# Optimization experiments

Measured on AMD Instinct MI355X. Metric: run time of the kernel, lower is better.

The kernel has to match this reference:

```python
import jax, jax.numpy as jnp
import numpy as np

N = 100000
E = 1000000
F_IN = 128
HID = 64
HEADS = 4
NC = 4


def setup_inputs() -> dict:
    key = jax.random.key(0)
    ks = jax.random.split(key, 24)
    s = 0.05
    inp = {
        "x": jax.random.normal(ks[0], (N, F_IN), jnp.float32),
        "edge_index": jax.random.randint(ks[1], (2, E), 0, N, jnp.int64 if jax.config.jax_enable_x64 else jnp.int32),
        "edge_weight": jax.random.uniform(ks[2], (E,), jnp.float32),
        "node_mask": jnp.ones((N,), jnp.bool_),
        # GCNConv: lin (no bias applied pre-propagate in math below; bias added after)
        "gcn_W": s * jax.random.normal(ks[3], (F_IN, HID), jnp.float32),
        "gcn_b": jnp.zeros((HID,), jnp.float32),
        "proj_W": s * jax.random.normal(ks[4], (F_IN, HID), jnp.float32),
        "proj_b": jnp.zeros((HID,), jnp.float32),
        "ln1_g": jnp.ones((HID,), jnp.float32), "ln1_b": jnp.zeros((HID,), jnp.float32),
        # GATv2Conv heads=4, concat=False: lin_l, lin_r -> [F, H*C], att [H, C], bias [C]
        "gat_Wl": s * jax.random.normal(ks[5], (HID, HEADS * HID), jnp.float32),
        "gat_Wr": s * jax.random.normal(ks[6], (HID, HEADS * HID), jnp.float32),
        "gat_att": s * jax.random.normal(ks[7], (HEADS, HID), jnp.float32),
        "gat_b": jnp.zeros((HID,), jnp.float32),
        "ln2_g": jnp.ones((HID,), jnp.float32), "ln2_b": jnp.zeros((HID,), jnp.float32),
        # SAGEConv: lin_l (neighbors, with bias), lin_r (root, no bias)
        "sage_Wl": s * jax.random.normal(ks[8], (HID, HID), jnp.float32),
        "sage_bl": jnp.zeros((HID,), jnp.float32),
        "sage_Wr": s * jax.random.normal(ks[9], (HID, HID), jnp.float32),
        "ln3_g": jnp.ones((HID,), jnp.float32), "ln3_b": jnp.zeros((HID,), jnp.float32),
        # edge MLP: Linear(2*HID+1, 32) -> ReLU -> Linear(32, 1)
        "emlp_W1": s * jax.random.normal(ks[10], (2 * HID + 1, 32), jnp.float32),
        "emlp_b1": jnp.zeros((32,), jnp.float32),
        "emlp_W2": s * jax.random.normal(ks[11], (32, 1), jnp.float32),
        "emlp_b2": jnp.zeros((1,), jnp.float32),
        # heads on JK-cat dim 3*HID
        "mort_W": s * jax.random.normal(ks[12], (3 * HID, 1), jnp.float32),
        "mort_b": jnp.zeros((1,), jnp.float32),
        "hours_W": s * jax.random.normal(ks[13], (3 * HID, 1), jnp.float32),
        "hours_b": jnp.zeros((1,), jnp.float32),
        "disc_W": s * jax.random.normal(ks[14], (3 * HID, NC), jnp.float32),
        "disc_b": jnp.zeros((NC,), jnp.float32),
    }
    return inp


def _ln(h, g, b, eps=1e-5):
    mu = jnp.mean(h, axis=-1, keepdims=True)
    var = jnp.mean(jnp.square(h - mu), axis=-1, keepdims=True)
    return (h - mu) * jax.lax.rsqrt(var + eps) * g + b


def reference(x, edge_index, edge_weight, node_mask,
              gcn_W, gcn_b, proj_W, proj_b, ln1_g, ln1_b,
              gat_Wl, gat_Wr, gat_att, gat_b, ln2_g, ln2_b,
              sage_Wl, sage_bl, sage_Wr, ln3_g, ln3_b,
              emlp_W1, emlp_b1, emlp_W2, emlp_b2,
              mort_W, mort_b, hours_W, hours_b, disc_W, disc_b):
    n = x.shape[0]
    src, dst = edge_index[0], edge_index[1]
    loop = jnp.arange(n, dtype=src.dtype)
    s2 = jnp.concatenate([src, loop])  # edges + self loops (GCN, GATv2)
    d2 = jnp.concatenate([dst, loop])

    # ---- GCNConv (normalized, self loops with weight 1) ----
    w2 = jnp.concatenate([edge_weight, jnp.ones((n,), x.dtype)])
    deg = jax.ops.segment_sum(w2, d2, num_segments=n)
    dinv = jnp.where(deg > 0, jax.lax.rsqrt(deg), 0.0)
    norm = dinv[s2] * w2 * dinv[d2]
    xw = x @ gcn_W  # [N, HID]
    gcn_out = jax.ops.segment_sum(norm[:, None] * xw[s2], d2, num_segments=n) + gcn_b
    h1 = jax.nn.relu(_ln(gcn_out, ln1_g, ln1_b))
    h_init = h1 + (x @ proj_W + proj_b)

    # ---- edge-gated edge MLP (recomputed weights; unused by later convs, kept for fidelity) ----
    feat = jnp.concatenate([h_init[src], h_init[dst], edge_weight[:, None]], axis=1)
    _new_ew = jax.nn.sigmoid((jax.nn.relu(feat @ emlp_W1 + emlp_b1) @ emlp_W2 + emlp_b2)[:, 0])

    # ---- GATv2Conv (heads=4, concat=False -> mean over heads, self loops) ----
    H, C = gat_att.shape
    xl = (h_init @ gat_Wl).reshape(n, H, C)
    xr = (h_init @ gat_Wr).reshape(n, H, C)
    e = jax.nn.leaky_relu(xl[s2] + xr[d2], 0.2)        # [E+N, H, C]
    score = jnp.einsum('ehc,hc->eh', e, gat_att)        # [E+N, H]
    smax = jax.ops.segment_max(score, d2, num_segments=n)
    ex = jnp.exp(score - smax[d2])
    den = jax.ops.segment_sum(ex, d2, num_segments=n)
    alpha = ex / den[d2]
    gat_out = jax.ops.segment_sum(alpha[:, :, None] * xl[s2], d2, num_segments=n)
    gat_out = jnp.mean(gat_out, axis=1) + gat_b
    h2 = jax.nn.relu(_ln(gat_out, ln2_g, ln2_b)) + h_init

    # ---- SAGEConv (mean aggregation, root weight, no self loops) ----
    nsum = jax.ops.segment_sum(h2[src], dst, num_segments=n)
    cnt = jax.ops.segment_sum(jnp.ones(src.shape, h2.dtype), dst, num_segments=n)
    nmean = nsum / jnp.maximum(cnt, 1.0)[:, None]
    sage_out = nmean @ sage_Wl + sage_bl + h2 @ sage_Wr
    h3 = jax.nn.relu(_ln(sage_out, ln3_g, ln3_b)) + h2

    # ---- JumpingKnowledge cat + masked readout + heads ----
    x_jk = jnp.concatenate([h_init, h2, h3], axis=1)  # [N, 3*HID]
    readout = jnp.where(node_mask[:, None], x_jk, 0.0)
    mort = (readout @ mort_W + mort_b)[:, 0]
    hours = (readout @ hours_W + hours_b)[:, 0]
    disc = readout @ disc_W + disc_b
    return mort, hours, disc
```

## Files before the change

### kernel.cpp

```cpp
#include <hip/hip_runtime.h>
#include <hip/hip_fp16.h>
#include <math.h>

#define N_NODES 100000
#define N_EDGES 1000000
#define F_IN    128
#define HID     64
#define HEADS   4
#define NCLS    4
#define SCAN_BLK 98
#define GEMM_NT 5

typedef _Float16 half8 __attribute__((ext_vector_type(8)));
typedef float f32x4 __attribute__((ext_vector_type(4)));

__device__ __forceinline__ float wsum(float v) {
#pragma unroll
  for (int o = 32; o > 0; o >>= 1) v += __shfl_xor(v, o, 64);
  return v;
}
struct Half4 { __half2 a, b; };
__device__ __forceinline__ float4 ld_half4(const __half* p) {
  Half4 h = *reinterpret_cast<const Half4*>(p);
  float2 f0 = __half22float2(h.a), f1 = __half22float2(h.b);
  return make_float4(f0.x, f0.y, f1.x, f1.y);
}
__device__ __forceinline__ int wave_node() {
  return __builtin_amdgcn_readfirstlane(blockIdx.x * 4 + (threadIdx.x >> 6));
}

__global__ void k_zero_cnt(int* __restrict__ cnt) {
  int i = blockIdx.x * 256 + threadIdx.x;
  if (i < N_NODES) cnt[i] = 0;
}
__global__ void k_hist(const int* __restrict__ dst, int* __restrict__ cnt) {
  int e = blockIdx.x * 256 + threadIdx.x;
  if (e < N_EDGES) atomicAdd(&cnt[dst[e]], 1);
}
__global__ __launch_bounds__(256) void k_scan1(const int* __restrict__ cnt,
                                               int* __restrict__ partial,
                                               int* __restrict__ bsum) {
  __shared__ int lds[256];
  int t = threadIdx.x;
  int base = blockIdx.x * 1024 + t * 4;
  int v0 = (base + 0 < N_NODES) ? cnt[base + 0] : 0;
  int v1 = (base + 1 < N_NODES) ? cnt[base + 1] : 0;
  int v2 = (base + 2 < N_NODES) ? cnt[base + 2] : 0;
  int v3 = (base + 3 < N_NODES) ? cnt[base + 3] : 0;
  int s = v0 + v1 + v2 + v3;
  lds[t] = s;
  __syncthreads();
  for (int o = 1; o < 256; o <<= 1) {
    int x = (t >= o) ? lds[t - o] : 0;
    __syncthreads();
    lds[t] += x;
    __syncthreads();
  }
  int excl = lds[t] - s;
  if (base + 0 < N_NODES) partial[base + 0] = excl;
  if (base + 1 < N_NODES) partial[base + 1] = excl + v0;
  if (base + 2 < N_NODES) partial[base + 2] = excl + v0 + v1;
  if (base + 3 < N_NODES) partial[base + 3] = excl + v0 + v1 + v2;
  if (t == 255) bsum[blockIdx.x] = lds[255];
}
__global__ void k_scan2(int* __restrict__ bsum) {
  __shared__ int lds[128];
  int t = threadIdx.x;
  int v = (t < SCAN_BLK) ? bsum[t] : 0;
  lds[t] = v;
  __syncthreads();
  for (int o = 1; o < 128; o <<= 1) {
    int x = (t >= o) ? lds[t - o] : 0;
    __syncthreads();
    lds[t] += x;
    __syncthreads();
  }
  if (t < SCAN_BLK) bsum[t] = lds[t] - v;
}
__global__ void k_scan3(const int* __restrict__ partial, const int* __restrict__ bsum,
                        int* __restrict__ row_ptr, int* __restrict__ cursor) {
  int i = blockIdx.x * 256 + threadIdx.x;
  if (i < N_NODES) {
    int v = partial[i] + bsum[i >> 10];
    row_ptr[i] = v;
    cursor[i] = v;
  }
  if (i == 0) row_ptr[N_NODES] = N_EDGES;
}
__global__ void k_fill(const int* __restrict__ src, const int* __restrict__ dst,
                       const float* __restrict__ ew, int* __restrict__ cursor,
                       int* __restrict__ csr_src, float* __restrict__ csr_w) {
  int e = blockIdx.x * 256 + threadIdx.x;
  if (e >= N_EDGES) return;
  int d = dst[e];
  int p = atomicAdd(&cursor[d], 1);
  csr_src[p] = src[e];
  csr_w[p] = ew[e];
}

__global__ __launch_bounds__(512) void k_in_gemm_mfma(
    const float* __restrict__ x, const float* __restrict__ gcn_W,
    const float* __restrict__ proj_W, const float* __restrict__ proj_b,
    __half* __restrict__ xw16, float* __restrict__ xp) {
  __shared__ __half at[16 * 136];
  int t = threadIdx.x;
  int w = t >> 6, lane = t & 63;
  int m = lane & 15, q = lane >> 4;
  int ncol = w * 16 + m;
  const float* W = (ncol < 64) ? gcn_W : proj_W;
  int nc = (ncol < 64) ? ncol : ncol - 64;
  half8 bf[4];
#pragma unroll
  for (int ch = 0; ch < 4; ++ch) {
    int kb = ch * 32 + q * 8;
#pragma unroll
    for (int j = 0; j < 8; ++j)
      bf[ch][j] = (_Float16)W[(kb + j) * 64 + nc];
  }
  float pb = (ncol >= 64) ? proj_b[nc] : 0.f;
  int nb0 = blockIdx.x * (16 * GEMM_NT);
  for (int nt = 0; nt < GEMM_NT; ++nt) {
    int nb = nb0 + nt * 16;
    {
      int row = t >> 5, col = (t & 31) * 4;
      float4 v = *reinterpret_cast<const float4*>(x + (size_t)(nb + row) * F_IN + col);
      __half2* d = reinterpret_cast<__half2*>(&at[row * 136 + col]);
      d[0] = __floats2half2_rn(v.x, v.y);
      d[1] = __floats2half2_rn(v.z, v.w);
    }
    __syncthreads();
    f32x4 acc = {0.f, 0.f, 0.f, 0.f};
#pragma unroll
    for (int ch = 0; ch < 4; ++ch) {
      half8 af = *reinterpret_cast<const half8*>(&at[m * 136 + ch * 32 + q * 8]);
      acc = __builtin_amdgcn_mfma_f32_16x16x32_f16(af, bf[ch], acc, 0, 0, 0);
    }
    if (ncol < 64) {
#pragma unroll
      for (int r = 0; r < 4; ++r)
        xw16[(size_t)(nb + q * 4 + r) * HID + nc] = __float2half(acc[r]);
    } else {
#pragma unroll
      for (int r = 0; r < 4; ++r)
        xp[(size_t)(nb + q * 4 + r) * HID + nc] = acc[r] + pb;
    }
    __syncthreads();
  }
}

__global__ void k_deg(const int* __restrict__ row_ptr, const float* __restrict__ csr_w,
                      float* __restrict__ dinv) {
  int n = blockIdx.x * 256 + threadIdx.x;
  if (n >= N_NODES) return;
  float deg = 1.0f;
  int end = row_ptr[n + 1];
  for (int i = row_ptr[n]; i < end; ++i) deg += csr_w[i];
  dinv[n] = rsqrtf(deg);
}

__global__ __launch_bounds__(256) void k_gcn_fused(
    const int* __restrict__ row_ptr, const int* __restrict__ csr_src,
    const float* __restrict__ csr_w, const float* __restrict__ dinv,
    const __half* __restrict__ xw16, const float* __restrict__ xp,
    const float* __restrict__ gcn_b, const float* __restrict__ g,
    const float* __restrict__ bb, float* __restrict__ h_init,
    __half* __restrict__ h_init16) {
  int n = wave_node();
  int lane = threadIdx.x & 63;
  float di = dinv[n];
  float acc = di * di * __half2float(xw16[(size_t)n * HID + lane]);
  int beg = row_ptr[n], end = row_ptr[n + 1];
  int i = beg;
  for (; i + 2 <= end; i += 2) {
    int s0 = __builtin_amdgcn_readfirstlane(csr_src[i]);
    int s1 = __builtin_amdgcn_readfirstlane(csr_src[i + 1]);
    float nrm0 = dinv[s0] * csr_w[i] * di;
    float nrm1 = dinv[s1] * csr_w[i + 1] * di;
    float v0 = __half2float(xw16[(size_t)s0 * HID + lane]);
    float v1 = __half2float(xw16[(size_t)s1 * HID + lane]);
    acc += nrm0 * v0 + nrm1 * v1;
  }
  if (i < end) {
    int s = __builtin_amdgcn_readfirstlane(csr_src[i]);
    float nrm = dinv[s] * csr_w[i] * di;
    acc += nrm * __half2float(xw16[(size_t)s * HID + lane]);
  }
  float v = acc + gcn_b[lane];
  float mu = wsum(v) * (1.f / HID);
  float dv = v - mu;
  float var = wsum(dv * dv) * (1.f / HID);
  float h = dv * rsqrtf(var + 1e-5f) * g[lane] + bb[lane];
  h = h > 0.f ? h : 0.f;
  float outv = h + xp[(size_t)n * HID + lane];
  h_init[(size_t)n * HID + lane] = outv;
  h_init16[(size_t)n * HID + lane] = __float2half(outv);
}

__global__ __launch_bounds__(512) void k_gat_gemm_mfma(
    const __half* __restrict__ h16, const float* __restrict__ Wl,
    const float* __restrict__ Wr, __half* __restrict__ xl, __half* __restrict__ xr) {
  __shared__ __half at[16 * 72];
  int t = threadIdx.x;
  int w = t >> 6, lane = t & 63;
  int m = lane & 15, q = lane >> 4;
  half8 bf[4][2];
#pragma unroll
  for (int tt = 0; tt < 4; ++tt) {
    int c = w * 16 + tt * 128 + m;
    const float* W = (c < 256) ? Wl : Wr;
    int nc = (c < 256) ? c : c - 256;
#pragma unroll
    for (int ch = 0; ch < 2; ++ch) {
      int kb = ch * 32 + q * 8;
#pragma unroll
      for (int j = 0; j < 8; ++j)
        bf[tt][ch][j] = (_Float16)W[(kb + j) * 256 + nc];
    }
  }
  int nb0 = blockIdx.x * (16 * GEMM_NT);
  for (int nt = 0; nt < GEMM_NT; ++nt) {
    int nb = nb0 + nt * 16;
    {
      int row = t >> 5, col = (t & 31) * 2;
      *reinterpret_cast<__half2*>(&at[row * 72 + col]) =
          *reinterpret_cast<const __half2*>(h16 + (size_t)(nb + row) * HID + col);
    }
    __syncthreads();
    half8 a0 = *reinterpret_cast<const half8*>(&at[m * 72 + q * 8]);
    half8 a1 = *reinterpret_cast<const half8*>(&at[m * 72 + 32 + q * 8]);
#pragma unroll
    for (int tt = 0; tt < 4; ++tt) {
      f32x4 acc = {0.f, 0.f, 0.f, 0.f};
      acc = __builtin_amdgcn_mfma_f32_16x16x32_f16(a0, bf[tt][0], acc, 0, 0, 0);
      acc = __builtin_amdgcn_mfma_f32_16x16x32_f16(a1, bf[tt][1], acc, 0, 0, 0);
      int c = w * 16 + tt * 128 + m;
      __half* out = (c < 256) ? (xl + c) : (xr + (c - 256));
#pragma unroll
      for (int r = 0; r < 4; ++r)
        out[(size_t)(nb + q * 4 + r) * 256] = __float2half(acc[r]);
    }
    __syncthreads();
  }
}

__global__ __launch_bounds__(256) void k_gat_fused(
    const int* __restrict__ row_ptr, const int* __restrict__ csr_src,
    const __half* __restrict__ xl, const __half* __restrict__ xr,
    const float* __restrict__ att, const float* __restrict__ gat_b,
    const float* __restrict__ g, const float* __restrict__ bb,
    const float* __restrict__ h_init, float* __restrict__ h2,
    __half* __restrict__ h2_16) {
  int n = wave_node();
  int lane = threadIdx.x & 63;
  float4 atv = *reinterpret_cast<const float4*>(att + lane * 4);
  float4 xrv = ld_half4(xr + (size_t)n * 256 + lane * 4);
  float4 xlv = ld_half4(xl + (size_t)n * 256 + lane * 4);

  float q, v;
  v = xlv.x + xrv.x; q  = (v > 0.f ? v : 0.2f * v) * atv.x;
  v = xlv.y + xrv.y; q += (v > 0.f ? v : 0.2f * v) * atv.y;
  v = xlv.z + xrv.z; q += (v > 0.f ? v : 0.2f * v) * atv.z;
  v = xlv.w + xrv.w; q += (v > 0.f ? v : 0.2f * v) * atv.w;
  q += __shfl_xor(q, 1); q += __shfl_xor(q, 2);
  q += __shfl_xor(q, 4); q += __shfl_xor(q, 8);
  float w = __expf(q);
  float den = w;
  float4 acc = make_float4(w * xlv.x, w * xlv.y, w * xlv.z, w * xlv.w);

  int beg = row_ptr[n], end = row_ptr[n + 1];
  int i = beg;
  for (; i + 2 <= end; i += 2) {
    int s0 = __builtin_amdgcn_readfirstlane(csr_src[i]);
    int s1 = __builtin_amdgcn_readfirstlane(csr_src[i + 1]);
    float4 a0 = ld_half4(xl + (size_t)s0 * 256 + lane * 4);
    float4 a1 = ld_half4(xl + (size_t)s1 * 256 + lane * 4);
    float q0, q1;
    v = a0.x + xrv.x; q0  = (v > 0.f ? v : 0.2f * v) * atv.x;
    v = a0.y + xrv.y; q0 += (v > 0.f ? v : 0.2f * v) * atv.y;
    v = a0.z + xrv.z; q0 += (v > 0.f ? v : 0.2f * v) * atv.z;
    v = a0.w + xrv.w; q0 += (v > 0.f ? v : 0.2f * v) * atv.w;
    v = a1.x + xrv.x; q1  = (v > 0.f ? v : 0.2f * v) * atv.x;
    v = a1.y + xrv.y; q1 += (v > 0.f ? v : 0.2f * v) * atv.y;
    v = a1.z + xrv.z; q1 += (v > 0.f ? v : 0.2f * v) * atv.z;
    v = a1.w + xrv.w; q1 += (v > 0.f ? v : 0.2f * v) * atv.w;
    q0 += __shfl_xor(q0, 1); q1 += __shfl_xor(q1, 1);
    q0 += __shfl_xor(q0, 2); q1 += __shfl_xor(q1, 2);
    q0 += __shfl_xor(q0, 4); q1 += __shfl_xor(q1, 4);
    q0 += __shfl_xor(q0, 8); q1 += __shfl_xor(q1, 8);
    float w0 = __expf(q0), w1 = __expf(q1);
    den += w0 + w1;
    acc.x += w0 * a0.x + w1 * a1.x;
    acc.y += w0 * a0.y + w1 * a1.y;
    acc.z += w0 * a0.z + w1 * a1.z;
    acc.w += w0 * a0.w + w1 * a1.w;
  }
  if (i < end) {
    int s0 = __builtin_amdgcn_readfirstlane(csr_src[i]);
    float4 a0 = ld_half4(xl + (size_t)s0 * 256 + lane * 4);
    v = a0.x + xrv.x; q  = (v > 0.f ? v : 0.2f * v) * atv.x;
    v = a0.y + xrv.y; q += (v > 0.f ? v : 0.2f * v) * atv.y;
    v = a0.z + xrv.z; q += (v > 0.f ? v : 0.2f * v) * atv.z;
    v = a0.w + xrv.w; q += (v > 0.f ? v : 0.2f * v) * atv.w;
    q += __shfl_xor(q, 1); q += __shfl_xor(q, 2);
    q += __shfl_xor(q, 4); q += __shfl_xor(q, 8);
    w = __expf(q);
    den += w;
    acc.x += w * a0.x; acc.y += w * a0.y;
    acc.z += w * a0.z; acc.w += w * a0.w;
  }
  float inv = 1.f / den;
  acc.x *= inv; acc.y *= inv; acc.z *= inv; acc.w *= inv;
  acc.x += __shfl_xor(acc.x, 16); acc.y += __shfl_xor(acc.y, 16);
  acc.z += __shfl_xor(acc.z, 16); acc.w += __shfl_xor(acc.w, 16);
  acc.x += __shfl_xor(acc.x, 32); acc.y += __shfl_xor(acc.y, 32);
  acc.z += __shfl_xor(acc.z, 32); acc.w += __shfl_xor(acc.w, 32);
  int srcl = lane >> 2;
  float t0 = __shfl(acc.x, srcl), t1 = __shfl(acc.y, srcl);
  float t2 = __shfl(acc.z, srcl), t3 = __shfl(acc.w, srcl);
  int r = lane & 3;
  float mean = (r == 0) ? t0 : (r == 1) ? t1 : (r == 2) ? t2 : t3;
  float val = mean * 0.25f + gat_b[lane];
  float mu = wsum(val) * (1.f / HID);
  float dv = val - mu;
  float var = wsum(dv * dv) * (1.f / HID);
  float h = dv * rsqrtf(var + 1e-5f) * g[lane] + bb[lane];
  h = h > 0.f ? h : 0.f;
  float outv = h + h_init[(size_t)n * HID + lane];
  h2[(size_t)n * HID + lane] = outv;
  h2_16[(size_t)n * HID + lane] = __float2half(outv);
}

__global__ __launch_bounds__(256) void k_sage_gather(
    const int* __restrict__ row_ptr, const int* __restrict__ csr_src,
    const __half* __restrict__ h2_16, float* __restrict__ nmean) {
  int n = wave_node();
  int lane = threadIdx.x & 63;
  int beg = row_ptr[n], end = row_ptr[n + 1];
  float sum = 0.f;
  int i = beg;
  for (; i + 2 <= end; i += 2) {
    int s0 = __builtin_amdgcn_readfirstlane(csr_src[i]);
    int s1 = __builtin_amdgcn_readfirstlane(csr_src[i + 1]);
    float v0 = __half2float(h2_16[(size_t)s0 * HID + lane]);
    float v1 = __half2float(h2_16[(size_t)s1 * HID + lane]);
    sum += v0 + v1;
  }
  if (i < end) {
    int s = __builtin_amdgcn_readfirstlane(csr_src[i]);
    sum += __half2float(h2_16[(size_t)s * HID + lane]);
  }
  nmean[(size_t)n * HID + lane] = sum / fmaxf((float)(end - beg), 1.f);
}

__global__ __launch_bounds__(64) void k_sage_gemm_ln(
    const float* __restrict__ nmean, const float* __restrict__ h2,
    const float* __restrict__ Wl, const float* __restrict__ Wr,
    const float* __restrict__ sage_bl, const float* __restrict__ g,
    const float* __restrict__ bb, float* __restrict__ h3) {
  __shared__ float nt[8][HID];
  __shared__ float ht[8][HID];
  int t = threadIdx.x;
  int n0 = blockIdx.x * 8;
  {
    const float4* ng = reinterpret_cast<const float4*>(nmean + (size_t)n0 * HID);
    const float4* hg = reinterpret_cast<const float4*>(h2 + (size_t)n0 * HID);
    float4* ns = reinterpret_cast<float4*>(&nt[0][0]);
    float4* hs = reinterpret_cast<float4*>(&ht[0][0]);
#pragma unroll
    for (int r = 0; r < 2; ++r) { ns[t + r * 64] = ng[t + r * 64]; hs[t + r * 64] = hg[t + r * 64]; }
  }
  __syncthreads();
  int f = t;
  float acc[8] = {0.f,0.f,0.f,0.f,0.f,0.f,0.f,0.f};
  for (int k = 0; k < HID; k += 4) {
    float wl0 = Wl[(k + 0) * HID + f], wr0 = Wr[(k + 0) * HID + f];
    float wl1 = Wl[(k + 1) * HID + f], wr1 = Wr[(k + 1) * HID + f];
    float wl2 = Wl[(k + 2) * HID + f], wr2 = Wr[(k + 2) * HID + f];
    float wl3 = Wl[(k + 3) * HID + f], wr3 = Wr[(k + 3) * HID + f];
#pragma unroll
    for (int j = 0; j < 8; ++j) {
      float4 nv = *reinterpret_cast<const float4*>(&nt[j][k]);
      float4 hv = *reinterpret_cast<const float4*>(&ht[j][k]);
      acc[j] += nv.x * wl0 + nv.y * wl1 + nv.z * wl2 + nv.w * wl3
              + hv.x * wr0 + hv.y * wr1 + hv.z * wr2 + hv.w * wr3;
    }
  }
  float blv = sage_bl[f], gv = g[f], bbv = bb[f];
#pragma unroll
  for (int j = 0; j < 8; ++j) {
    float v = acc[j] + blv;
    float mu = wsum(v) * (1.f / HID);
    float dv = v - mu;
    float var = wsum(dv * dv) * (1.f / HID);
    float h = dv * rsqrtf(var + 1e-5f) * gv + bbv;
    h = h > 0.f ? h : 0.f;
    h3[(size_t)(n0 + j) * HID + f] = h + ht[j][f];
  }
}

__global__ __launch_bounds__(256) void k_heads(
    const float* __restrict__ h_init, const float* __restrict__ h2,
    const float* __restrict__ h3, const int* __restrict__ mask,
    const float* __restrict__ mort_W, const float* __restrict__ mort_b,
    const float* __restrict__ hours_W, const float* __restrict__ hours_b,
    const float* __restrict__ disc_W, const float* __restrict__ disc_b,
    float* __restrict__ out) {
  int n = wave_node();
  int lane = threadIdx.x & 63;
  float m = (mask[n] != 0) ? 1.f : 0.f;
  size_t base = (size_t)n * HID;
  float v0 = h_init[base + lane] * m;
  float v1 = h2[base + lane] * m;
  float v2 = h3[base + lane] * m;
  float pm = v0 * mort_W[lane] + v1 * mort_W[64 + lane] + v2 * mort_W[128 + lane];
  float ph = v0 * hours_W[lane] + v1 * hours_W[64 + lane] + v2 * hours_W[128 + lane];
  float d0 = v0 * disc_W[lane * 4 + 0] + v1 * disc_W[(64 + lane) * 4 + 0] + v2 * disc_W[(128 + lane) * 4 + 0];
  float d1 = v0 * disc_W[lane * 4 + 1] + v1 * disc_W[(64 + lane) * 4 + 1] + v2 * disc_W[(128 + lane) * 4 + 1];
  float d2 = v0 * disc_W[lane * 4 + 2] + v1 * disc_W[(64 + lane) * 4 + 2] + v2 * disc_W[(128 + lane) * 4 + 2];
  float d3 = v0 * disc_W[lane * 4 + 3] + v1 * disc_W[(64 + lane) * 4 + 3] + v2 * disc_W[(128 + lane) * 4 + 3];
  pm = wsum(pm); ph = wsum(ph);
  d0 = wsum(d0); d1 = wsum(d1); d2 = wsum(d2); d3 = wsum(d3);
  if (lane == 0) {
    out[n] = pm + mort_b[0];
    out[N_NODES + n] = ph + hours_b[0];
    float* dd = out + 2 * N_NODES + (size_t)n * 4;
    dd[0] = d0 + disc_b[0];
    dd[1] = d1 + disc_b[1];
    dd[2] = d2 + disc_b[2];
    dd[3] = d3 + disc_b[3];
  }
}

extern "C" void kernel_launch(void* const* d_in, const int* in_sizes, int n_in,
                              void* d_out, int out_size, void* d_ws, size_t ws_size,
                              hipStream_t stream) {
  const float* x       = (const float*)d_in[0];
  const int*   ei      = (const int*)d_in[1];
  const float* ew      = (const float*)d_in[2];
  const int*   mask    = (const int*)d_in[3];
  const float* gcn_W   = (const float*)d_in[4];
  const float* gcn_b   = (const float*)d_in[5];
  const float* proj_W  = (const float*)d_in[6];
  const float* proj_b  = (const float*)d_in[7];
  const float* ln1_g   = (const float*)d_in[8];
  const float* ln1_b   = (const float*)d_in[9];
  const float* gat_Wl  = (const float*)d_in[10];
  const float* gat_Wr  = (const float*)d_in[11];
  const float* gat_att = (const float*)d_in[12];
  const float* gat_b   = (const float*)d_in[13];
  const float* ln2_g   = (const float*)d_in[14];
  const float* ln2_b   = (const float*)d_in[15];
  const float* sage_Wl = (const float*)d_in[16];
  const float* sage_bl = (const float*)d_in[17];
  const float* sage_Wr = (const float*)d_in[18];
  const float* ln3_g   = (const float*)d_in[19];
  const float* ln3_b   = (const float*)d_in[20];
  const float* mort_W  = (const float*)d_in[25];
  const float* mort_b  = (const float*)d_in[26];
  const float* hours_W = (const float*)d_in[27];
  const float* hours_b = (const float*)d_in[28];
  const float* disc_W  = (const float*)d_in[29];
  const float* disc_b  = (const float*)d_in[30];

  const int* src = ei;
  const int* dst = ei + N_EDGES;
  float* out = (float*)d_out;

  float* ws = (float*)d_ws;
  const size_t F = (size_t)N_NODES * HID;
  float* h_init = ws;
  float* h2     = ws + 1 * F;
  float* h3     = ws + 2 * F;
  float* xp     = h3;
  __half* xl    = (__half*)(ws + 3 * F);
  __half* xw16  = xl;
  float* nmean  = ws + 3 * F;
  __half* xr    = (__half*)(ws + 3 * F + (size_t)N_NODES * 128);
  __half* h2_16 = (__half*)(ws + 3 * F + (size_t)N_NODES * 256);
  __half* h_init16 = (__half*)(ws + 3 * F + (size_t)N_NODES * 288);
  float* tail   = ws + 3 * F + (size_t)N_NODES * 320;
  int*   csr_src = (int*)tail;           tail += N_EDGES;
  float* csr_w   = tail;                 tail += N_EDGES;
  int*   row_ptr = (int*)tail;           tail += N_NODES + 64;
  int*   cursor  = (int*)tail;           tail += N_NODES;
  int*   cnt     = (int*)tail;           tail += N_NODES;
  int*   partial = (int*)tail;           tail += N_NODES;
  int*   bsum    = (int*)tail;           tail += 128;
  float* dinv    = tail;

  const int GE = (N_EDGES + 255) / 256;
  const int GN = (N_NODES + 255) / 256;
  const int GB = N_NODES / (16 * GEMM_NT);

  k_zero_cnt<<<GN, 256, 0, stream>>>(cnt);
  k_hist<<<GE, 256, 0, stream>>>(dst, cnt);
  k_scan1<<<SCAN_BLK, 256, 0, stream>>>(cnt, partial, bsum);
  k_scan2<<<1, 128, 0, stream>>>(bsum);
  k_scan3<<<GN, 256, 0, stream>>>(partial, bsum, row_ptr, cursor);
  k_fill<<<GE, 256, 0, stream>>>(src, dst, ew, cursor, csr_src, csr_w);

  k_in_gemm_mfma<<<GB, 512, 0, stream>>>(x, gcn_W, proj_W, proj_b, xw16, xp);
  k_deg<<<GN, 256, 0, stream>>>(row_ptr, csr_w, dinv);
  k_gcn_fused<<<N_NODES / 4, 256, 0, stream>>>(row_ptr, csr_src, csr_w, dinv, xw16,
                                               xp, gcn_b, ln1_g, ln1_b, h_init, h_init16);

  k_gat_gemm_mfma<<<GB, 512, 0, stream>>>(h_init16, gat_Wl, gat_Wr, xl, xr);
  k_gat_fused<<<N_NODES / 4, 256, 0, stream>>>(row_ptr, csr_src, xl, xr, gat_att,
                                               gat_b, ln2_g, ln2_b, h_init, h2, h2_16);

  k_sage_gather<<<N_NODES / 4, 256, 0, stream>>>(row_ptr, csr_src, h2_16, nmean);
  k_sage_gemm_ln<<<N_NODES / 8, 64, 0, stream>>>(nmean, h2, sage_Wl, sage_Wr,
                                                 sage_bl, ln3_g, ln3_b, h3);

  k_heads<<<N_NODES / 4, 256, 0, stream>>>(h_init, h2, h3, mask, mort_W, mort_b,
                                           hours_W, hours_b, disc_W, disc_b, out);
}
```

Measured before the change: 600.2 us.

## Drop fp32 node-feature copies, compute GAT scores in packed fp16, unroll gathers by four

h_init and h2 are no longer stored in fp32. Downstream kernels (GAT residual, SAGE root term, heads) read the existing fp16 copies instead, which cuts write and read traffic. The GATv2 edge score is now computed with packed half2 arithmetic: leaky ReLU is written as 0.6x+0.4|x| and the attention dot product uses the fdot2 instruction. The GCN and SAGE neighbor-gather loops are unrolled to four edges to expose more memory-level parallelism. The trade-off is lower precision in the residuals, in the heads inputs and in the attention logits, which may affect numerical accuracy.

```diff
diff --git a/kernel.cpp b/kernel.cpp
--- a/kernel.cpp
+++ b/kernel.cpp
@@ -12,6 +12,7 @@
 #define GEMM_NT 5
 
 typedef _Float16 half8 __attribute__((ext_vector_type(8)));
+typedef _Float16 fp16x2 __attribute__((ext_vector_type(2)));
 typedef float f32x4 __attribute__((ext_vector_type(4)));
 
 __device__ __forceinline__ float wsum(float v) {
@@ -24,6 +25,30 @@
   Half4 h = *reinterpret_cast<const Half4*>(p);
   float2 f0 = __half22float2(h.a), f1 = __half22float2(h.b);
   return make_float4(f0.x, f0.y, f1.x, f1.y);
+}
+__device__ __forceinline__ __half2 absh2(__half2 v) {
+  unsigned u; __builtin_memcpy(&u, &v, 4);
+  u &= 0x7FFF7FFFu;
+  __half2 r; __builtin_memcpy(&r, &u, 4);
+  return r;
+}
+__device__ __forceinline__ float fdot2f(__half2 a, __half2 b, float c) {
+#if defined(__has_builtin) && __has_builtin(__builtin_amdgcn_fdot2)
+  fp16x2 av, bv;
+  __builtin_memcpy(&av, &a, 4); __builtin_memcpy(&bv, &b, 4);
+  return __builtin_amdgcn_fdot2(av, bv, c, false);
+#else
+  float2 af = __half22float2(a), bf = __half22float2(b);
+  return c + af.x * bf.x + af.y * bf.y;
+#endif
+}
+__device__ __forceinline__ float edge_score(Half4 A, __half2 Ra, __half2 Rb,
+                                            __half2 at0, __half2 at1,
+                                            __half2 c06, __half2 c04) {
+  __half2 t0 = __hadd2(A.a, Ra), t1 = __hadd2(A.b, Rb);
+  __half2 l0 = __hfma2(t0, c06, __hmul2(absh2(t0), c04));
+  __half2 l1 = __hfma2(t1, c06, __hmul2(absh2(t1), c04));
+  return fdot2f(l1, at1, fdot2f(l0, at0, 0.f));
 }
 __device__ __forceinline__ int wave_node() {
   return __builtin_amdgcn_readfirstlane(blockIdx.x * 4 + (threadIdx.x >> 6));
@@ -163,24 +188,29 @@
     const float* __restrict__ csr_w, const float* __restrict__ dinv,
     const __half* __restrict__ xw16, const float* __restrict__ xp,
     const float* __restrict__ gcn_b, const float* __restrict__ g,
-    const float* __restrict__ bb, float* __restrict__ h_init,
-    __half* __restrict__ h_init16) {
+    const float* __restrict__ bb, __half* __restrict__ h_init16) {
   int n = wave_node();
   int lane = threadIdx.x & 63;
   float di = dinv[n];
   float acc = di * di * __half2float(xw16[(size_t)n * HID + lane]);
   int beg = row_ptr[n], end = row_ptr[n + 1];
   int i = beg;
-  for (; i + 2 <= end; i += 2) {
+  for (; i + 4 <= end; i += 4) {
     int s0 = __builtin_amdgcn_readfirstlane(csr_src[i]);
     int s1 = __builtin_amdgcn_readfirstlane(csr_src[i + 1]);
+    int s2 = __builtin_amdgcn_readfirstlane(csr_src[i + 2]);
+    int s3 = __builtin_amdgcn_readfirstlane(csr_src[i + 3]);
     float nrm0 = dinv[s0] * csr_w[i] * di;
     float nrm1 = dinv[s1] * csr_w[i + 1] * di;
+    float nrm2 = dinv[s2] * csr_w[i + 2] * di;
+    float nrm3 = dinv[s3] * csr_w[i + 3] * di;
     float v0 = __half2float(xw16[(size_t)s0 * HID + lane]);
     float v1 = __half2float(xw16[(size_t)s1 * HID + lane]);
-    acc += nrm0 * v0 + nrm1 * v1;
-  }
-  if (i < end) {
+    float v2 = __half2float(xw16[(size_t)s2 * HID + lane]);
+    float v3 = __half2float(xw16[(size_t)s3 * HID + lane]);
+    acc += nrm0 * v0 + nrm1 * v1 + nrm2 * v2 + nrm3 * v3;
+  }
+  for (; i < end; ++i) {
     int s = __builtin_amdgcn_readfirstlane(csr_src[i]);
     float nrm = dinv[s] * csr_w[i] * di;
     acc += nrm * __half2float(xw16[(size_t)s * HID + lane]);
@@ -191,9 +221,7 @@
   float var = wsum(dv * dv) * (1.f / HID);
   float h = dv * rsqrtf(var + 1e-5f) * g[lane] + bb[lane];
   h = h > 0.f ? h : 0.f;
-  float outv = h + xp[(size_t)n * HID + lane];
-  h_init[(size_t)n * HID + lane] = outv;
-  h_init16[(size_t)n * HID + lane] = __float2half(outv);
+  h_init16[(size_t)n * HID + lane] = __float2half(h + xp[(size_t)n * HID + lane]);
 }
 
 __global__ __launch_bounds__(512) void k_gat_gemm_mfma(
@@ -248,65 +276,58 @@
     const __half* __restrict__ xl, const __half* __restrict__ xr,
     const float* __restrict__ att, const float* __restrict__ gat_b,
     const float* __restrict__ g, const float* __restrict__ bb,
-    const float* __restrict__ h_init, float* __restrict__ h2,
-    __half* __restrict__ h2_16) {
+    const __half* __restrict__ h_init16, __half* __restrict__ h2_16) {
   int n = wave_node();
   int lane = threadIdx.x & 63;
+  const __half2 c06 = __float2half2_rn(0.6f);
+  const __half2 c04 = __float2half2_rn(0.4f);
   float4 atv = *reinterpret_cast<const float4*>(att + lane * 4);
-  float4 xrv = ld_half4(xr + (size_t)n * 256 + lane * 4);
-  float4 xlv = ld_half4(xl + (size_t)n * 256 + lane * 4);
-
-  float q, v;
-  v = xlv.x + xrv.x; q  = (v > 0.f ? v : 0.2f * v) * atv.x;
-  v = xlv.y + xrv.y; q += (v > 0.f ? v : 0.2f * v) * atv.y;
-  v = xlv.z + xrv.z; q += (v > 0.f ? v : 0.2f * v) * atv.z;
-  v = xlv.w + xrv.w; q += (v > 0.f ? v : 0.2f * v) * atv.w;
+  __half2 at0 = __floats2half2_rn(atv.x, atv.y);
+  __half2 at1 = __floats2half2_rn(atv.z, atv.w);
+  Half4 R = *reinterpret_cast<const Half4*>(xr + (size_t)n * 256 + lane * 4);
+  Half4 S = *reinterpret_cast<const Half4*>(xl + (size_t)n * 256 + lane * 4);
+
+  float q = edge_score(S, R.a, R.b, at0, at1, c06, c04);
   q += __shfl_xor(q, 1); q += __shfl_xor(q, 2);
   q += __shfl_xor(q, 4); q += __shfl_xor(q, 8);
   float w = __expf(q);
   float den = w;
-  float4 acc = make_float4(w * xlv.x, w * xlv.y, w * xlv.z, w * xlv.w);
+  float2 f0 = __half22float2(S.a), f1 = __half22float2(S.b);
+  float4 acc = make_float4(w * f0.x, w * f0.y, w * f1.x, w * f1.y);
 
   int beg = row_ptr[n], end = row_ptr[n + 1];
   int i = beg;
   for (; i + 2 <= end; i += 2) {
     int s0 = __builtin_amdgcn_readfirstlane(csr_src[i]);
     int s1 = __builtin_amdgcn_readfirstlane(csr_src[i + 1]);
-    float4 a0 = ld_half4(xl + (size_t)s0 * 256 + lane * 4);
-    float4 a1 = ld_half4(xl + (size_t)s1 * 256 + lane * 4);
-    float q0, q1;
-    v = a0.x + xrv.x; q0  = (v > 0.f ? v : 0.2f * v) * atv.x;
-    v = a0.y + xrv.y; q0 += (v > 0.f ? v : 0.2f * v) * atv.y;
-    v = a0.z + xrv.z; q0 += (v > 0.f ? v : 0.2f * v) * atv.z;
-    v = a0.w + xrv.w; q0 += (v > 0.f ? v : 0.2f * v) * atv.w;
-    v = a1.x + xrv.x; q1  = (v > 0.f ? v : 0.2f * v) * atv.x;
-    v = a1.y + xrv.y; q1 += (v > 0.f ? v : 0.2f * v) * atv.y;
-    v = a1.z + xrv.z; q1 += (v > 0.f ? v : 0.2f * v) * atv.z;
-    v = a1.w + xrv.w; q1 += (v > 0.f ? v : 0.2f * v) * atv.w;
+    Half4 A0 = *reinterpret_cast<const Half4*>(xl + (size_t)s0 * 256 + lane * 4);
+    Half4 A1 = *reinterpret_cast<const Half4*>(xl + (size_t)s1 * 256 + lane * 4);
+    float q0 = edge_score(A0, R.a, R.b, at0, at1, c06, c04);
+    float q1 = edge_score(A1, R.a, R.b, at0, at1, c06, c04);
     q0 += __shfl_xor(q0, 1); q1 += __shfl_xor(q1, 1);
     q0 += __shfl_xor(q0, 2); q1 += __shfl_xor(q1, 2);
     q0 += __shfl_xor(q0, 4); q1 += __shfl_xor(q1, 4);
     q0 += __shfl_xor(q0, 8); q1 += __shfl_xor(q1, 8);
     float w0 = __expf(q0), w1 = __expf(q1);
     den += w0 + w1;
-    acc.x += w0 * a0.x + w1 * a1.x;
-    acc.y += w0 * a0.y + w1 * a1.y;
-    acc.z += w0 * a0.z + w1 * a1.z;
-    acc.w += w0 * a0.w + w1 * a1.w;
+    float2 a00 = __half22float2(A0.a), a01 = __half22float2(A0.b);
+    float2 a10 = __half22float2(A1.a), a11 = __half22float2(A1.b);
+    acc.x += w0 * a00.x + w1 * a10.x;
+    acc.y += w0 * a00.y + w1 * a10.y;
+    acc.z += w0 * a01.x + w1 * a11.x;
+    acc.w += w0 * a01.y + w1 * a11.y;
   }
   if (i < end) {
     int s0 = __builtin_amdgcn_readfirstlane(csr_src[i]);
-    float4 a0 = ld_half4(xl + (size_t)s0 * 256 + lane * 4);
-    v = a0.x + xrv.x; q  = (v > 0.f ? v : 0.2f * v) * atv.x;
-    v = a0.y + xrv.y; q += (v > 0.f ? v : 0.2f * v) * atv.y;
-    v = a0.z + xrv.z; q += (v > 0.f ? v : 0.2f * v) * atv.z;
-    v = a0.w + xrv.w; q += (v > 0.f ? v : 0.2f * v) * atv.w;
+    Half4 A0 = *reinterpret_cast<const Half4*>(xl + (size_t)s0 * 256 + lane * 4);
+    q = edge_score(A0, R.a, R.b, at0, at1, c06, c04);
     q += __shfl_xor(q, 1); q += __shfl_xor(q, 2);
     q += __shfl_xor(q, 4); q += __shfl_xor(q, 8);
     w = __expf(q);
     den += w;
-    acc.x += w * a0.x; acc.y += w * a0.y;
-    acc.z += w * a0.z; acc.w += w * a0.w;
+    float2 a00 = __half22float2(A0.a), a01 = __half22float2(A0.b);
+    acc.x += w * a00.x; acc.y += w * a00.y;
+    acc.z += w * a01.x; acc.w += w * a01.y;
   }
   float inv = 1.f / den;
   acc.x *= inv; acc.y *= inv; acc.z *= inv; acc.w *= inv;
@@ -325,8 +346,7 @@
   float var = wsum(dv * dv) * (1.f / HID);
   float h = dv * rsqrtf(var + 1e-5f) * g[lane] + bb[lane];
   h = h > 0.f ? h : 0.f;
-  float outv = h + h_init[(size_t)n * HID + lane];
-  h2[(size_t)n * HID + lane] = outv;
+  float outv = h + __half2float(h_init16[(size_t)n * HID + lane]);
   h2_16[(size_t)n * HID + lane] = __float2half(outv);
 }
 
@@ -338,14 +358,18 @@
   int beg = row_ptr[n], end = row_ptr[n + 1];
   float sum = 0.f;
   int i = beg;
-  for (; i + 2 <= end; i += 2) {
+  for (; i + 4 <= end; i += 4) {
     int s0 = __builtin_amdgcn_readfirstlane(csr_src[i]);
     int s1 = __builtin_amdgcn_readfirstlane(csr_src[i + 1]);
+    int s2 = __builtin_amdgcn_readfirstlane(csr_src[i + 2]);
+    int s3 = __builtin_amdgcn_readfirstlane(csr_src[i + 3]);
     float v0 = __half2float(h2_16[(size_t)s0 * HID + lane]);
     float v1 = __half2float(h2_16[(size_t)s1 * HID + lane]);
-    sum += v0 + v1;
-  }
-  if (i < end) {
+    float v2 = __half2float(h2_16[(size_t)s2 * HID + lane]);
+    float v3 = __half2float(h2_16[(size_t)s3 * HID + lane]);
+    sum += v0 + v1 + v2 + v3;
+  }
+  for (; i < end; ++i) {
     int s = __builtin_amdgcn_readfirstlane(csr_src[i]);
     sum += __half2float(h2_16[(size_t)s * HID + lane]);
   }
@@ -353,7 +377,7 @@
 }
 
 __global__ __launch_bounds__(64) void k_sage_gemm_ln(
-    const float* __restrict__ nmean, const float* __restrict__ h2,
+    const float* __restrict__ nmean, const __half* __restrict__ h2_16,
     const float* __restrict__ Wl, const float* __restrict__ Wr,
     const float* __restrict__ sage_bl, const float* __restrict__ g,
     const float* __restrict__ bb, float* __restrict__ h3) {
@@ -363,11 +387,18 @@
   int n0 = blockIdx.x * 8;
   {
     const float4* ng = reinterpret_cast<const float4*>(nmean + (size_t)n0 * HID);
-    const float4* hg = reinterpret_cast<const float4*>(h2 + (size_t)n0 * HID);
     float4* ns = reinterpret_cast<float4*>(&nt[0][0]);
-    float4* hs = reinterpret_cast<float4*>(&ht[0][0]);
-#pragma unroll
-    for (int r = 0; r < 2; ++r) { ns[t + r * 64] = ng[t + r * 64]; hs[t + r * 64] = hg[t + r * 64]; }
+    ns[t] = ng[t];
+    ns[t + 64] = ng[t + 64];
+    const __half* hp = h2_16 + (size_t)n0 * HID + t * 8;
+    Half4 p0 = *reinterpret_cast<const Half4*>(hp);
+    Half4 p1 = *reinterpret_cast<const Half4*>(hp + 4);
+    float* dsth = &ht[0][0] + t * 8;
+    float2 f;
+    f = __half22float2(p0.a); dsth[0] = f.x; dsth[1] = f.y;
+    f = __half22float2(p0.b); dsth[2] = f.x; dsth[3] = f.y;
+    f = __half22float2(p1.a); dsth[4] = f.x; dsth[5] = f.y;
+    f = __half22float2(p1.b); dsth[6] = f.x; dsth[7] = f.y;
   }
   __syncthreads();
   int f = t;
@@ -399,7 +430,7 @@
 }
 
 __global__ __launch_bounds__(256) void k_heads(
-    const float* __restrict__ h_init, const float* __restrict__ h2,
+    const __half* __restrict__ h_init16, const __half* __restrict__ h2_16,
     const float* __restrict__ h3, const int* __restrict__ mask,
     const float* __restrict__ mort_W, const float* __restrict__ mort_b,
     const float* __restrict__ hours_W, const float* __restrict__ hours_b,
@@ -409,8 +440,8 @@
   int lane = threadIdx.x & 63;
   float m = (mask[n] != 0) ? 1.f : 0.f;
   size_t base = (size_t)n * HID;
-  float v0 = h_init[base + lane] * m;
-  float v1 = h2[base + lane] * m;
+  float v0 = __half2float(h_init16[base + lane]) * m;
+  float v1 = __half2float(h2_16[base + lane]) * m;
   float v2 = h3[base + lane] * m;
   float pm = v0 * mort_W[lane] + v1 * mort_W[64 + lane] + v2 * mort_W[128 + lane];
   float ph = v0 * hours_W[lane] + v1 * hours_W[64 + lane] + v2 * hours_W[128 + lane];
@@ -468,8 +499,6 @@
 
   float* ws = (float*)d_ws;
   const size_t F = (size_t)N_NODES * HID;
-  float* h_init = ws;
-  float* h2     = ws + 1 * F;
   float* h3     = ws + 2 * F;
   float* xp     = h3;
   __half* xl    = (__half*)(ws + 3 * F);
@@ -502,16 +531,16 @@
   k_in_gemm_mfma<<<GB, 512, 0, stream>>>(x, gcn_W, proj_W, proj_b, xw16, xp);
   k_deg<<<GN, 256, 0, stream>>>(row_ptr, csr_w, dinv);
   k_gcn_fused<<<N_NODES / 4, 256, 0, stream>>>(row_ptr, csr_src, csr_w, dinv, xw16,
-                                               xp, gcn_b, ln1_g, ln1_b, h_init, h_init16);
+                                               xp, gcn_b, ln1_g, ln1_b, h_init16);
 
   k_gat_gemm_mfma<<<GB, 512, 0, stream>>>(h_init16, gat_Wl, gat_Wr, xl, xr);
   k_gat_fused<<<N_NODES / 4, 256, 0, stream>>>(row_ptr, csr_src, xl, xr, gat_att,
-                                               gat_b, ln2_g, ln2_b, h_init, h2, h2_16);
+                                               gat_b, ln2_g, ln2_b, h_init16, h2_16);
 
   k_sage_gather<<<N_NODES / 4, 256, 0, stream>>>(row_ptr, csr_src, h2_16, nmean);
-  k_sage_gemm_ln<<<N_NODES / 8, 64, 0, stream>>>(nmean, h2, sage_Wl, sage_Wr,
+  k_sage_gemm_ln<<<N_NODES / 8, 64, 0, stream>>>(nmean, h2_16, sage_Wl, sage_Wr,
                                                  sage_bl, ln3_g, ln3_b, h3);
 
-  k_heads<<<N_NODES / 4, 256, 0, stream>>>(h_init, h2, h3, mask, mort_W, mort_b,
+  k_heads<<<N_NODES / 4, 256, 0, stream>>>(h_init16, h2_16, h3, mask, mort_W, mort_b,
                                            hours_W, hours_b, disc_W, disc_b, out);
 }
```

After: 575.2 us. 1.04x faster.
